# Kernel optimization log

Measured on AMD Instinct MI355X. Metric: run time of the kernel, lower is better.

Reference implementation:

```python
import jax, jax.numpy as jnp
import numpy as np

B, S, D = 4, 2048, 1024
H = 16
HD = D // H
FF = 4096
EPS = 1e-5

def _layernorm(x, g, b):
    mu = jnp.mean(x, axis=-1, keepdims=True)
    var = jnp.mean(jnp.square(x - mu), axis=-1, keepdims=True)
    return (x - mu) * jax.lax.rsqrt(var + EPS) * g + b

def setup_inputs() -> dict:
    key = jax.random.key(0)
    ks = jax.random.split(key, 12)
    s_attn = 1.0 / np.sqrt(D)
    s_ff1 = 1.0 / np.sqrt(D)
    s_ff2 = 1.0 / np.sqrt(FF)
    return {
        "x": jax.random.normal(ks[0], (B, S, D), jnp.float32),
        "ln1_g": jnp.ones((D,), jnp.float32),
        "ln1_b": jnp.zeros((D,), jnp.float32),
        "ln2_g": jnp.ones((D,), jnp.float32),
        "ln2_b": jnp.zeros((D,), jnp.float32),
        "Wq": jax.random.normal(ks[1], (D, D), jnp.float32) * s_attn,
        "Wk": jax.random.normal(ks[2], (D, D), jnp.float32) * s_attn,
        "Wv": jax.random.normal(ks[3], (D, D), jnp.float32) * s_attn,
        "Wo": jax.random.normal(ks[4], (D, D), jnp.float32) * s_attn,
        "W1": jax.random.normal(ks[5], (D, FF), jnp.float32) * s_ff1,
        "b1": jnp.zeros((FF,), jnp.float32),
        "W2": jax.random.normal(ks[6], (FF, D), jnp.float32) * s_ff2,
        "b2": jnp.zeros((D,), jnp.float32),
    }

def reference(x, ln1_g, ln1_b, ln2_g, ln2_b, Wq, Wk, Wv, Wo, W1, b1, W2, b2):
    # pre-LN self-attention (y = x), mask=None, dropout=0, attn proj bias=False
    h = _layernorm(x, ln1_g, ln1_b)                      # [B,S,D]
    q = (h @ Wq).reshape(B, S, H, HD).transpose(0, 2, 1, 3)  # [B,H,S,HD]
    k = (h @ Wk).reshape(B, S, H, HD).transpose(0, 2, 1, 3)
    v = (h @ Wv).reshape(B, S, H, HD).transpose(0, 2, 1, 3)
    scores = jnp.einsum('bhqd,bhkd->bhqk', q, k) / np.sqrt(HD)  # [B,H,S,S]
    attn = jax.nn.softmax(scores, axis=-1)
    o = jnp.einsum('bhqk,bhkd->bhqd', attn, v)           # [B,H,S,HD]
    o = o.transpose(0, 2, 1, 3).reshape(B, S, D) @ Wo
    x = x + o
    h2 = _layernorm(x, ln2_g, ln2_b)
    ff = jax.nn.relu(h2 @ W1 + b1) @ W2 + b2             # note: second FC also has relu per FC default
    ff = jax.nn.relu(ff)
    return x + ff
```

## Files before the change

### kernel.cpp

```cpp
#include <hip/hip_runtime.h>
#include <hip/hip_bf16.h>
#include <cstdint>
#include <cstddef>

typedef unsigned short u16;
typedef unsigned int u32;
typedef __bf16 bf16x2 __attribute__((ext_vector_type(2)));
typedef __bf16 bf16x8 __attribute__((ext_vector_type(8)));
typedef float f32x4 __attribute__((ext_vector_type(4)));

#define NB 4
#define NS 2048
#define ND 1024
#define NH 16
#define NHD 64
#define NFF 4096
#define CSC 0.18033688011112042f

#if __has_builtin(__builtin_amdgcn_exp2f)
#define EXP2(x) __builtin_amdgcn_exp2f(x)
#else
#define EXP2(x) exp2f(x)
#endif

__device__ __forceinline__ u16 f2b(float f) {
  union { bf16x2 h; u32 u; } v;
  v.h[0] = (__bf16)f; v.h[1] = (__bf16)f;
  return (u16)(v.u & 0xFFFF);
}
__device__ __forceinline__ u32 pack2(float a, float b) {
  union { bf16x2 h; u32 u; } v;
  v.h[0] = (__bf16)a; v.h[1] = (__bf16)b;
  return v.u;
}

__device__ __forceinline__ void async_copy16(const u16* g, u16* l) {
  __builtin_amdgcn_global_load_lds(
      (const __attribute__((address_space(1))) void*)(const void*)g,
      (__attribute__((address_space(3))) void*)(void*)l, 16, 0, 0);
}

template <int N> __device__ __forceinline__ void vmw() {
  if constexpr (N == 0) asm volatile("s_waitcnt vmcnt(0)" ::: "memory");
  else if constexpr (N == 6) asm volatile("s_waitcnt vmcnt(6)" ::: "memory");
}

__global__ __launch_bounds__(256) void transpose_f2b(const float* __restrict__ in,
                                                     u16* __restrict__ out,
                                                     int R, int C) {
  __shared__ float tile[32][33];
  const int bx = blockIdx.x * 32;
  const int by = blockIdx.y * 32;
  const int tx = threadIdx.x & 31, ty = threadIdx.x >> 5;
#pragma unroll
  for (int i = 0; i < 32; i += 8)
    tile[ty + i][tx] = in[(size_t)(by + ty + i) * C + bx + tx];
  __syncthreads();
#pragma unroll
  for (int i = 0; i < 32; i += 8)
    out[(size_t)(bx + ty + i) * R + by + tx] = f2b(tile[tx][ty + i]);
}

__global__ __launch_bounds__(256) void ln_kernel(const float* __restrict__ xin,
                                                 const float* __restrict__ g,
                                                 const float* __restrict__ b,
                                                 u16* __restrict__ out) {
  const int row = blockIdx.x;
  const int tid = threadIdx.x;
  const float* p = xin + (size_t)row * ND;
  float v[4];
#pragma unroll
  for (int i = 0; i < 4; i++) v[i] = p[tid + 256 * i];
  float s = 0.f, ss = 0.f;
#pragma unroll
  for (int i = 0; i < 4; i++) { s += v[i]; ss += v[i] * v[i]; }
  for (int off = 32; off > 0; off >>= 1) {
    s += __shfl_down(s, off);
    ss += __shfl_down(ss, off);
  }
  __shared__ float r0[4], r1[4];
  const int w = tid >> 6;
  if ((tid & 63) == 0) { r0[w] = s; r1[w] = ss; }
  __syncthreads();
  s = r0[0] + r0[1] + r0[2] + r0[3];
  ss = r1[0] + r1[1] + r1[2] + r1[3];
  const float mu = s * (1.f / ND);
  const float var = ss * (1.f / ND) - mu * mu;
  const float rstd = rsqrtf(var + 1e-5f);
  u16* o = out + (size_t)row * ND;
#pragma unroll
  for (int i = 0; i < 4; i++) {
    const int c = tid + 256 * i;
    o[c] = f2b((v[i] - mu) * rstd * g[c] + b[c]);
  }
}

template <int OUT_MODE, int RES_MODE, bool BIAS, bool RELU>
__global__ __launch_bounds__(256) void gemm_bt(const u16* __restrict__ A,
                                               const u16* __restrict__ Bt,
                                               const float* __restrict__ bias,
                                               const float* __restrict__ res,
                                               void* __restrict__ out,
                                               u16* __restrict__ outK,
                                               u16* __restrict__ outV,
                                               int M, int N, int K) {
  __shared__ __align__(16) u16 lA[2][128 * 64];
  __shared__ __align__(16) u16 lB[2][128 * 64];
  const int tid = threadIdx.x;
  const int bm = blockIdx.y * 128, bn = blockIdx.x * 128;
  const int w = tid >> 6, lane = tid & 63, quad = lane >> 4, l16 = lane & 15;
  const int wm = (w & 1) * 64, wn = (w >> 1) * 64;
  const int sw = l16 & 7;

  f32x4 acc[4][4];
#pragma unroll
  for (int i = 0; i < 4; i++)
#pragma unroll
    for (int j = 0; j < 4; j++) acc[i][j] = (f32x4){0.f, 0.f, 0.f, 0.f};

  const int srow = w * 8 + (lane >> 3);
  const int sch = (lane & 7) ^ ((lane >> 3) & 7);
  const u16* Ap = A + (size_t)(bm + srow) * K + sch * 8;
  const u16* Bp = Bt + (size_t)(bn + srow) * K + sch * 8;
  const int NT = K >> 6;

#pragma unroll
  for (int c = 0; c < 4; c++)
    async_copy16(Ap + (size_t)c * 32 * K, &lA[0][(c * 32 + w * 8) * 64]);
#pragma unroll
  for (int c = 0; c < 4; c++)
    async_copy16(Bp + (size_t)c * 32 * K, &lB[0][(c * 32 + w * 8) * 64]);

  for (int kt = 0; kt < NT; ++kt) {
    const int cur = kt & 1;
    __syncthreads();
    if (kt + 1 < NT) {
      const size_t koff = (size_t)(kt + 1) * 64;
#pragma unroll
      for (int c = 0; c < 4; c++)
        async_copy16(Ap + (size_t)c * 32 * K + koff,
                     &lA[cur ^ 1][(c * 32 + w * 8) * 64]);
#pragma unroll
      for (int c = 0; c < 4; c++)
        async_copy16(Bp + (size_t)c * 32 * K + koff,
                     &lB[cur ^ 1][(c * 32 + w * 8) * 64]);
    }
    const u16* lAc = lA[cur];
    const u16* lBc = lB[cur];
#pragma unroll
    for (int x = 0; x < 2; x++) {
      bf16x8 af[4], bf[4];
#pragma unroll
      for (int i = 0; i < 4; i++)
        af[i] = *(const bf16x8*)&lAc[(wm + i * 16 + l16) * 64 + ((x * 4 + quad) ^ sw) * 8];
#pragma unroll
      for (int j = 0; j < 4; j++)
        bf[j] = *(const bf16x8*)&lBc[(wn + j * 16 + l16) * 64 + ((x * 4 + quad) ^ sw) * 8];
#pragma unroll
      for (int i = 0; i < 4; i++)
#pragma unroll
        for (int j = 0; j < 4; j++)
          acc[i][j] = __builtin_amdgcn_mfma_f32_16x16x32_bf16(af[i], bf[j], acc[i][j], 0, 0, 0);
    }
  }

  if constexpr (OUT_MODE == 3) {
    const int m0 = bm + wm;
#pragma unroll
    for (int i = 0; i < 4; i++) {
#pragma unroll
      for (int j = 0; j < 4; j++) {
        const int n = bn + wn + j * 16 + l16;
        const int mB = m0 + i * 16 + quad * 4;
        const int bb = mB >> 11, s = mB & 2047;
        if (bn < 1024) {
          const int hh = n >> 6, hd = n & 63;
          u16* o = (u16*)out + (((size_t)(bb * NH + hh) * NS + s) * NHD + hd);
#pragma unroll
          for (int r = 0; r < 4; r++) o[(size_t)r * NHD] = f2b(acc[i][j][r] * CSC);
        } else if (bn < 2048) {
          const int nk = n - 1024;
          const int hh = nk >> 6, hd = nk & 63;
          u16* o = outK + (((size_t)(bb * NH + hh) * NS + s) * NHD + hd);
#pragma unroll
          for (int r = 0; r < 4; r++) o[(size_t)r * NHD] = f2b(acc[i][j][r]);
        } else {
          const int nv = n - 2048;
          const int hh = nv >> 6, hd = nv & 63;
          uint2 pk = make_uint2(pack2(acc[i][j][0], acc[i][j][1]),
                                pack2(acc[i][j][2], acc[i][j][3]));
          *(uint2*)&outV[((size_t)(bb * NH + hh) * NHD + hd) * NS + s] = pk;
        }
      }
    }
  } else {
#pragma unroll
    for (int i = 0; i < 4; i++) {
#pragma unroll
      for (int r = 0; r < 4; r++) {
        const int m = bm + wm + i * 16 + quad * 4 + r;
#pragma unroll
        for (int j = 0; j < 4; j++) {
          const int n = bn + wn + j * 16 + l16;
          float vv = acc[i][j][r];
          if constexpr (BIAS) vv += bias[n];
          if constexpr (RELU) vv = fmaxf(vv, 0.f);
          if constexpr (RES_MODE == 1) vv += res[(size_t)m * N + n];
          if constexpr (OUT_MODE == 0) {
            ((u16*)out)[(size_t)m * N + n] = f2b(vv);
          } else {
            ((float*)out)[(size_t)m * N + n] = vv;
          }
        }
      }
    }
  }
}

template <bool BIAS, bool RELU>
__global__ __launch_bounds__(512, 2) void gemm_8ph(const u16* __restrict__ A,
                                                   const u16* __restrict__ Bt,
                                                   const float* __restrict__ bias,
                                                   u16* __restrict__ out,
                                                   int M, int N, int K) {
  __shared__ __align__(16) u16 lA[2][256 * 64];
  __shared__ __align__(16) u16 lB[2][256 * 64];
  const int tid = threadIdx.x;
  const int w = tid >> 6, lane = tid & 63, quad = lane >> 4, l16 = lane & 15;
  const int sw = l16 & 7;
  const int wr = w >> 2, wc = w & 3;

  const int nb = gridDim.x, chunk = nb >> 3;
  const int wg = ((int)blockIdx.x & 7) * chunk + ((int)blockIdx.x >> 3);
  const int nby = M >> 8;
  const int bx = wg / nby, by = wg % nby;
  const int bm = by * 256, bn = bx * 256;

  f32x4 acc[8][4];
#pragma unroll
  for (int i = 0; i < 8; i++)
#pragma unroll
    for (int j = 0; j < 4; j++) acc[i][j] = (f32x4){0.f, 0.f, 0.f, 0.f};

  const int srow = w * 8 + (lane >> 3);
  const int sch = (lane & 7) ^ ((lane >> 3) & 7);
  const u16* Ap = A + (size_t)(bm + srow) * K + sch * 8;
  const u16* Bp = Bt + (size_t)(bn + srow) * K + sch * 8;
  const int NT = K >> 6;

  auto stA = [&](int t, int h) {
    async_copy16(Ap + (size_t)(h * 64) * K + (size_t)t * 64,
                 &lA[t & 1][(h * 64 + w * 8) * 64]);
  };
  auto stB = [&](int t, int h) {
    async_copy16(Bp + (size_t)(h * 64) * K + (size_t)t * 64,
                 &lB[t & 1][(h * 64 + w * 8) * 64]);
  };

  stA(0, 0); stA(0, 1); stA(0, 2); stA(0, 3);
  stB(0, 0); stB(0, 1); stB(0, 2); stB(0, 3);
  stB(1, 0); stB(1, 1); stB(1, 2); stB(1, 3);
  stA(1, 0); stA(1, 2);
  vmw<6>();
  __builtin_amdgcn_s_barrier();
  __builtin_amdgcn_sched_barrier(0);

  for (int kt = 0; kt < NT; ++kt) {
    const u16* lAc = lA[kt & 1];
    const u16* lBc = lB[kt & 1];
    bf16x8 bfr[4][2];
#pragma unroll
    for (int p = 0; p < 4; ++p) {
      bf16x8 af[2][2];
#pragma unroll
      for (int ii = 0; ii < 2; ii++)
#pragma unroll
        for (int x = 0; x < 2; x++)
          af[ii][x] = *(const bf16x8*)&lAc[(wr * 128 + (p * 2 + ii) * 16 + l16) * 64 +
                                           ((x * 4 + quad) ^ sw) * 8];
      if (p == 0) {
#pragma unroll
        for (int j = 0; j < 4; j++)
#pragma unroll
          for (int x = 0; x < 2; x++)
            bfr[j][x] = *(const bf16x8*)&lBc[(wc * 64 + j * 16 + l16) * 64 +
                                             ((x * 4 + quad) ^ sw) * 8];
        if (kt + 1 < NT) { stA(kt + 1, 1); stA(kt + 1, 3); }
      } else if (p == 1) {
        if (kt + 2 < NT) { stB(kt + 2, 0); stB(kt + 2, 1); }
      } else if (p == 2) {
        if (kt + 2 < NT) { stB(kt + 2, 2); stB(kt + 2, 3); }
      } else {
        if (kt + 2 < NT) { stA(kt + 2, 0); stA(kt + 2, 2); }
      }
      __builtin_amdgcn_s_barrier();
      __builtin_amdgcn_sched_barrier(0);
      __builtin_amdgcn_s_setprio(1);
#pragma unroll
      for (int ii = 0; ii < 2; ii++)
#pragma unroll
        for (int j = 0; j < 4; j++)
#pragma unroll
          for (int x = 0; x < 2; x++)
            acc[p * 2 + ii][j] = __builtin_amdgcn_mfma_f32_16x16x32_bf16(
                af[ii][x], bfr[j][x], acc[p * 2 + ii][j], 0, 0, 0);
      __builtin_amdgcn_s_setprio(0);
      if (p == 3) {
        if (kt + 2 < NT) {
          vmw<6>();
          __builtin_amdgcn_sched_barrier(0);
        } else if (kt + 1 < NT) {
          vmw<0>();
          __builtin_amdgcn_sched_barrier(0);
        }
      }
      __builtin_amdgcn_s_barrier();
      __builtin_amdgcn_sched_barrier(0);
    }
  }

#pragma unroll
  for (int i = 0; i < 8; i++) {
#pragma unroll
    for (int r = 0; r < 4; r++) {
      const int m = bm + wr * 128 + i * 16 + quad * 4 + r;
#pragma unroll
      for (int j = 0; j < 4; j++) {
        const int n = bn + wc * 64 + j * 16 + l16;
        float vv = acc[i][j][r];
        if constexpr (BIAS) vv += bias[n];
        if constexpr (RELU) vv = fmaxf(vv, 0.f);
        out[(size_t)m * N + n] = f2b(vv);
      }
    }
  }
}

#define OSTR 72
__global__ __launch_bounds__(256, 4) void attn_kernel(const u16* __restrict__ Q,
                                                      const u16* __restrict__ K,
                                                      const u16* __restrict__ VT,
                                                      u16* __restrict__ O) {
  __shared__ __align__(16) u16 lK[128 * 64];
  __shared__ __align__(16) u16 lV[64 * 128];
  const int tid = threadIdx.x;
  const int w = tid >> 6, lane = tid & 63, quad = lane >> 4, l16 = lane & 15;
  const int sw = l16 & 7;

  const int bid = blockIdx.x;
  const int xcd = bid & 7, slot = bid >> 3;
  const int bh = xcd + 8 * (slot >> 5);
  const int q0 = (slot & 31) * 64;
  const size_t base = (size_t)bh * NS * NHD;

  const u16* qrow = Q + base + (size_t)(q0 + w * 16 + l16) * NHD;
  bf16x8 qf[2];
  qf[0] = *(const bf16x8*)(qrow + quad * 8);
  qf[1] = *(const bf16x8*)(qrow + 32 + quad * 8);

  const int krow = w * 8 + (lane >> 3);
  const int kch = (lane & 7) ^ ((lane >> 3) & 7);
  const int vrow = w * 4 + (lane >> 4);
  const int vch = (lane & 15) ^ (vrow & 7);
  const u16* kp = K + base + (size_t)krow * 64 + kch * 8;
  const u16* vp = VT + base + (size_t)vrow * NS + vch * 8;

  float l_i = 0.f;
  f32x4 oa[4];
#pragma unroll
  for (int jo = 0; jo < 4; jo++) oa[jo] = (f32x4){0.f, 0.f, 0.f, 0.f};

  for (int kt = 0; kt < NS / 128; ++kt) {
    __syncthreads();
#pragma unroll
    for (int c = 0; c < 4; c++)
      async_copy16(kp + (size_t)c * 32 * 64, &lK[(c * 32 + w * 8) * 64]);
#pragma unroll
    for (int c = 0; c < 4; c++)
      async_copy16(vp + (size_t)c * 16 * NS, &lV[(c * 16 + w * 4) * 128]);
    __syncthreads();
    kp += 128 * 64;
    vp += 128;

    f32x4 sc[8];
#pragma unroll
    for (int j = 0; j < 8; j++) sc[j] = (f32x4){0.f, 0.f, 0.f, 0.f};
#pragma unroll
    for (int x = 0; x < 2; x++)
#pragma unroll
      for (int j = 0; j < 8; j++) {
        bf16x8 kf = *(const bf16x8*)&lK[(j * 16 + l16) * 64 + ((x * 4 + quad) ^ sw) * 8];
        sc[j] = __builtin_amdgcn_mfma_f32_16x16x32_bf16(kf, qf[x], sc[j], 0, 0, 0);
      }

    float rsum = 0.f;
#pragma unroll
    for (int j = 0; j < 8; j++) {
#pragma unroll
      for (int r = 0; r < 4; r++) sc[j][r] = EXP2(sc[j][r]);
      rsum += (sc[j][0] + sc[j][1]) + (sc[j][2] + sc[j][3]);
    }
    rsum += __shfl_xor(rsum, 16);
    rsum += __shfl_xor(rsum, 32);
    l_i += rsum;

#pragma unroll
    for (int x = 0; x < 4; x++) {
      u32 A0 = pack2(sc[2 * x][0], sc[2 * x][1]);
      u32 A1 = pack2(sc[2 * x][2], sc[2 * x][3]);
      u32 B0 = pack2(sc[2 * x + 1][0], sc[2 * x + 1][1]);
      u32 B1 = pack2(sc[2 * x + 1][2], sc[2 * x + 1][3]);
      asm("v_permlane32_swap_b32 %0, %1" : "+v"(A0), "+v"(B0));
      asm("v_permlane32_swap_b32 %0, %1" : "+v"(A1), "+v"(B1));
      asm("v_permlane16_swap_b32 %0, %1" : "+v"(A0), "+v"(B0));
      asm("v_permlane16_swap_b32 %0, %1" : "+v"(A1), "+v"(B1));
      union { u32 u[4]; bf16x8 h; } bq;
      bq.u[0] = A0; bq.u[1] = A1; bq.u[2] = B0; bq.u[3] = B1;
#pragma unroll
      for (int jo = 0; jo < 4; jo++) {
        bf16x8 av = *(const bf16x8*)&lV[(jo * 16 + l16) * 128 + ((x * 4 + quad) ^ sw) * 8];
        oa[jo] = __builtin_amdgcn_mfma_f32_16x16x32_bf16(av, bq.h, oa[jo], 0, 0, 0);
      }
    }
  }

  __syncthreads();
  const float inv = 1.f / l_i;
  u16* lo = &lK[w * 16 * OSTR];
#pragma unroll
  for (int jo = 0; jo < 4; jo++)
#pragma unroll
    for (int pr = 0; pr < 2; pr++)
      *(u32*)&lo[l16 * OSTR + jo * 16 + quad * 4 + pr * 2] =
          pack2(oa[jo][2 * pr] * inv, oa[jo][2 * pr + 1] * inv);

  const int bb = bh >> 4, hh = bh & 15;
#pragma unroll
  for (int t = 0; t < 2; t++) {
    const int row = t * 8 + (lane >> 3);
    const int seg = lane & 7;
    bf16x8 ov = *(const bf16x8*)&lo[row * OSTR + seg * 8];
    const int srow = q0 + w * 16 + row;
    *(int4*)&O[((size_t)bb * NS + srow) * ND + hh * 64 + seg * 8] = *(int4*)&ov;
  }
}

extern "C" void kernel_launch(void* const* d_in, const int* in_sizes, int n_in,
                              void* d_out, int out_size, void* d_ws, size_t ws_size,
                              hipStream_t stream) {
  (void)in_sizes; (void)n_in; (void)out_size; (void)ws_size;
  const float* x = (const float*)d_in[0];
  const float* ln1g = (const float*)d_in[1];
  const float* ln1b = (const float*)d_in[2];
  const float* ln2g = (const float*)d_in[3];
  const float* ln2b = (const float*)d_in[4];
  const float* Wq = (const float*)d_in[5];
  const float* Wk = (const float*)d_in[6];
  const float* Wv = (const float*)d_in[7];
  const float* Wo = (const float*)d_in[8];
  const float* W1 = (const float*)d_in[9];
  const float* b1 = (const float*)d_in[10];
  const float* W2 = (const float*)d_in[11];
  const float* b2 = (const float*)d_in[12];

  u16* ws = (u16*)d_ws;
  u16* h     = ws;
  u16* WqkvT = ws + (size_t)8  * 1048576;
  u16* WoT   = ws + (size_t)11 * 1048576;
  u16* W1T   = ws + (size_t)12 * 1048576;
  u16* W2T   = ws + (size_t)16 * 1048576;
  u16* qb    = ws + (size_t)20 * 1048576;
  u16* kb    = ws + (size_t)28 * 1048576;
  u16* vt    = ws + (size_t)36 * 1048576;
  u16* ob    = ws + (size_t)44 * 1048576;
  float* x2  = (float*)(ws + (size_t)52 * 1048576);
  u16* ff    = qb;
  u16* h2    = h;

  const int M = NB * NS;

  transpose_f2b<<<dim3(32, 32), 256, 0, stream>>>(Wq, WqkvT, ND, ND);
  transpose_f2b<<<dim3(32, 32), 256, 0, stream>>>(Wk, WqkvT + (size_t)1024 * 1024, ND, ND);
  transpose_f2b<<<dim3(32, 32), 256, 0, stream>>>(Wv, WqkvT + (size_t)2048 * 1024, ND, ND);
  transpose_f2b<<<dim3(32, 32), 256, 0, stream>>>(Wo, WoT, ND, ND);
  transpose_f2b<<<dim3(128, 32), 256, 0, stream>>>(W1, W1T, ND, NFF);
  transpose_f2b<<<dim3(32, 128), 256, 0, stream>>>(W2, W2T, NFF, ND);

  ln_kernel<<<M, 256, 0, stream>>>(x, ln1g, ln1b, h);

  gemm_bt<3, 0, false, false><<<dim3(24, 64), 256, 0, stream>>>(
      h, WqkvT, nullptr, nullptr, qb, kb, vt, M, 3072, ND);

  attn_kernel<<<dim3(2048), 256, 0, stream>>>(qb, kb, vt, ob);

  gemm_bt<2, 1, false, false><<<dim3(8, 64), 256, 0, stream>>>(
      ob, WoT, nullptr, x, x2, nullptr, nullptr, M, ND, ND);

  ln_kernel<<<M, 256, 0, stream>>>(x2, ln2g, ln2b, h2);

  gemm_8ph<true, true><<<512, 512, 0, stream>>>(h2, W1T, b1, ff, M, NFF, ND);

  gemm_bt<2, 1, true, true><<<dim3(8, 64), 256, 0, stream>>>(
      ff, W2T, b2, x2, d_out, nullptr, nullptr, M, ND, NFF);
}
```

Baseline: 507.7 us.

## Route all GEMMs through 256x256 eight-phase kernel and merge weight transposes

Removes the simpler 128x128 double-buffered gemm_bt kernel. The QKV, output-projection and FFN2 GEMMs now run on the generalized 256x256 eight-phase pipelined gemm_8ph kernel, which gains the head-split QKV epilogue and residual/fp32 output modes. The four square weight transposes are also merged into one launch. The larger tiles should raise data reuse and MFMA efficiency, but the N=1024 GEMMs only launch 128 blocks, which may underfill the GPU.

After: 567.9 us. +11.9%, slower.

```diff
diff --git a/kernel.cpp b/kernel.cpp
--- a/kernel.cpp
+++ b/kernel.cpp
@@ -43,6 +43,28 @@
 template <int N> __device__ __forceinline__ void vmw() {
   if constexpr (N == 0) asm volatile("s_waitcnt vmcnt(0)" ::: "memory");
   else if constexpr (N == 6) asm volatile("s_waitcnt vmcnt(6)" ::: "memory");
+}
+
+__global__ __launch_bounds__(256) void transpose4_f2b(const float* __restrict__ Wq,
+                                                      const float* __restrict__ Wk,
+                                                      const float* __restrict__ Wv,
+                                                      const float* __restrict__ Wo,
+                                                      u16* __restrict__ WqkvT,
+                                                      u16* __restrict__ WoT) {
+  __shared__ float tile[32][33];
+  const int z = blockIdx.z;
+  const float* in = (z == 0) ? Wq : (z == 1) ? Wk : (z == 2) ? Wv : Wo;
+  u16* out = (z < 3) ? WqkvT + (size_t)z * 1024 * 1024 : WoT;
+  const int bx = blockIdx.x * 32;
+  const int by = blockIdx.y * 32;
+  const int tx = threadIdx.x & 31, ty = threadIdx.x >> 5;
+#pragma unroll
+  for (int i = 0; i < 32; i += 8)
+    tile[ty + i][tx] = in[(size_t)(by + ty + i) * 1024 + bx + tx];
+  __syncthreads();
+#pragma unroll
+  for (int i = 0; i < 32; i += 8)
+    out[(size_t)(bx + ty + i) * 1024 + by + tx] = f2b(tile[tx][ty + i]);
 }
 
 __global__ __launch_bounds__(256) void transpose_f2b(const float* __restrict__ in,
@@ -96,132 +118,13 @@
 }
 
 template <int OUT_MODE, int RES_MODE, bool BIAS, bool RELU>
-__global__ __launch_bounds__(256) void gemm_bt(const u16* __restrict__ A,
-                                               const u16* __restrict__ Bt,
-                                               const float* __restrict__ bias,
-                                               const float* __restrict__ res,
-                                               void* __restrict__ out,
-                                               u16* __restrict__ outK,
-                                               u16* __restrict__ outV,
-                                               int M, int N, int K) {
-  __shared__ __align__(16) u16 lA[2][128 * 64];
-  __shared__ __align__(16) u16 lB[2][128 * 64];
-  const int tid = threadIdx.x;
-  const int bm = blockIdx.y * 128, bn = blockIdx.x * 128;
-  const int w = tid >> 6, lane = tid & 63, quad = lane >> 4, l16 = lane & 15;
-  const int wm = (w & 1) * 64, wn = (w >> 1) * 64;
-  const int sw = l16 & 7;
-
-  f32x4 acc[4][4];
-#pragma unroll
-  for (int i = 0; i < 4; i++)
-#pragma unroll
-    for (int j = 0; j < 4; j++) acc[i][j] = (f32x4){0.f, 0.f, 0.f, 0.f};
-
-  const int srow = w * 8 + (lane >> 3);
-  const int sch = (lane & 7) ^ ((lane >> 3) & 7);
-  const u16* Ap = A + (size_t)(bm + srow) * K + sch * 8;
-  const u16* Bp = Bt + (size_t)(bn + srow) * K + sch * 8;
-  const int NT = K >> 6;
-
-#pragma unroll
-  for (int c = 0; c < 4; c++)
-    async_copy16(Ap + (size_t)c * 32 * K, &lA[0][(c * 32 + w * 8) * 64]);
-#pragma unroll
-  for (int c = 0; c < 4; c++)
-    async_copy16(Bp + (size_t)c * 32 * K, &lB[0][(c * 32 + w * 8) * 64]);
-
-  for (int kt = 0; kt < NT; ++kt) {
-    const int cur = kt & 1;
-    __syncthreads();
-    if (kt + 1 < NT) {
-      const size_t koff = (size_t)(kt + 1) * 64;
-#pragma unroll
-      for (int c = 0; c < 4; c++)
-        async_copy16(Ap + (size_t)c * 32 * K + koff,
-                     &lA[cur ^ 1][(c * 32 + w * 8) * 64]);
-#pragma unroll
-      for (int c = 0; c < 4; c++)
-        async_copy16(Bp + (size_t)c * 32 * K + koff,
-                     &lB[cur ^ 1][(c * 32 + w * 8) * 64]);
-    }
-    const u16* lAc = lA[cur];
-    const u16* lBc = lB[cur];
-#pragma unroll
-    for (int x = 0; x < 2; x++) {
-      bf16x8 af[4], bf[4];
-#pragma unroll
-      for (int i = 0; i < 4; i++)
-        af[i] = *(const bf16x8*)&lAc[(wm + i * 16 + l16) * 64 + ((x * 4 + quad) ^ sw) * 8];
-#pragma unroll
-      for (int j = 0; j < 4; j++)
-        bf[j] = *(const bf16x8*)&lBc[(wn + j * 16 + l16) * 64 + ((x * 4 + quad) ^ sw) * 8];
-#pragma unroll
-      for (int i = 0; i < 4; i++)
-#pragma unroll
-        for (int j = 0; j < 4; j++)
-          acc[i][j] = __builtin_amdgcn_mfma_f32_16x16x32_bf16(af[i], bf[j], acc[i][j], 0, 0, 0);
-    }
-  }
-
-  if constexpr (OUT_MODE == 3) {
-    const int m0 = bm + wm;
-#pragma unroll
-    for (int i = 0; i < 4; i++) {
-#pragma unroll
-      for (int j = 0; j < 4; j++) {
-        const int n = bn + wn + j * 16 + l16;
-        const int mB = m0 + i * 16 + quad * 4;
-        const int bb = mB >> 11, s = mB & 2047;
-        if (bn < 1024) {
-          const int hh = n >> 6, hd = n & 63;
-          u16* o = (u16*)out + (((size_t)(bb * NH + hh) * NS + s) * NHD + hd);
-#pragma unroll
-          for (int r = 0; r < 4; r++) o[(size_t)r * NHD] = f2b(acc[i][j][r] * CSC);
-        } else if (bn < 2048) {
-          const int nk = n - 1024;
-          const int hh = nk >> 6, hd = nk & 63;
-          u16* o = outK + (((size_t)(bb * NH + hh) * NS + s) * NHD + hd);
-#pragma unroll
-          for (int r = 0; r < 4; r++) o[(size_t)r * NHD] = f2b(acc[i][j][r]);
-        } else {
-          const int nv = n - 2048;
-          const int hh = nv >> 6, hd = nv & 63;
-          uint2 pk = make_uint2(pack2(acc[i][j][0], acc[i][j][1]),
-                                pack2(acc[i][j][2], acc[i][j][3]));
-          *(uint2*)&outV[((size_t)(bb * NH + hh) * NHD + hd) * NS + s] = pk;
-        }
-      }
-    }
-  } else {
-#pragma unroll
-    for (int i = 0; i < 4; i++) {
-#pragma unroll
-      for (int r = 0; r < 4; r++) {
-        const int m = bm + wm + i * 16 + quad * 4 + r;
-#pragma unroll
-        for (int j = 0; j < 4; j++) {
-          const int n = bn + wn + j * 16 + l16;
-          float vv = acc[i][j][r];
-          if constexpr (BIAS) vv += bias[n];
-          if constexpr (RELU) vv = fmaxf(vv, 0.f);
-          if constexpr (RES_MODE == 1) vv += res[(size_t)m * N + n];
-          if constexpr (OUT_MODE == 0) {
-            ((u16*)out)[(size_t)m * N + n] = f2b(vv);
-          } else {
-            ((float*)out)[(size_t)m * N + n] = vv;
-          }
-        }
-      }
-    }
-  }
-}
-
-template <bool BIAS, bool RELU>
 __global__ __launch_bounds__(512, 2) void gemm_8ph(const u16* __restrict__ A,
                                                    const u16* __restrict__ Bt,
                                                    const float* __restrict__ bias,
-                                                   u16* __restrict__ out,
+                                                   const float* __restrict__ res,
+                                                   void* __restrict__ out,
+                                                   u16* __restrict__ outK,
+                                                   u16* __restrict__ outV,
                                                    int M, int N, int K) {
   __shared__ __align__(16) u16 lA[2][256 * 64];
   __shared__ __align__(16) u16 lB[2][256 * 64];
@@ -319,18 +222,54 @@
     }
   }
 
-#pragma unroll
-  for (int i = 0; i < 8; i++) {
-#pragma unroll
-    for (int r = 0; r < 4; r++) {
-      const int m = bm + wr * 128 + i * 16 + quad * 4 + r;
+  if constexpr (OUT_MODE == 3) {
+    const int m0 = bm + wr * 128;
+#pragma unroll
+    for (int i = 0; i < 8; i++) {
 #pragma unroll
       for (int j = 0; j < 4; j++) {
         const int n = bn + wc * 64 + j * 16 + l16;
-        float vv = acc[i][j][r];
-        if constexpr (BIAS) vv += bias[n];
-        if constexpr (RELU) vv = fmaxf(vv, 0.f);
-        out[(size_t)m * N + n] = f2b(vv);
+        const int mB = m0 + i * 16 + quad * 4;
+        const int bb = mB >> 11, s = mB & 2047;
+        if (n < 1024) {
+          const int hh = n >> 6, hd = n & 63;
+          u16* o = (u16*)out + (((size_t)(bb * NH + hh) * NS + s) * NHD + hd);
+#pragma unroll
+          for (int r = 0; r < 4; r++) o[(size_t)r * NHD] = f2b(acc[i][j][r] * CSC);
+        } else if (n < 2048) {
+          const int nk = n - 1024;
+          const int hh = nk >> 6, hd = nk & 63;
+          u16* o = outK + (((size_t)(bb * NH + hh) * NS + s) * NHD + hd);
+#pragma unroll
+          for (int r = 0; r < 4; r++) o[(size_t)r * NHD] = f2b(acc[i][j][r]);
+        } else {
+          const int nv = n - 2048;
+          const int hh = nv >> 6, hd = nv & 63;
+          uint2 pk = make_uint2(pack2(acc[i][j][0], acc[i][j][1]),
+                                pack2(acc[i][j][2], acc[i][j][3]));
+          *(uint2*)&outV[((size_t)(bb * NH + hh) * NHD + hd) * NS + s] = pk;
+        }
+      }
+    }
+  } else {
+#pragma unroll
+    for (int i = 0; i < 8; i++) {
+#pragma unroll
+      for (int r = 0; r < 4; r++) {
+        const int m = bm + wr * 128 + i * 16 + quad * 4 + r;
+#pragma unroll
+        for (int j = 0; j < 4; j++) {
+          const int n = bn + wc * 64 + j * 16 + l16;
+          float vv = acc[i][j][r];
+          if constexpr (BIAS) vv += bias[n];
+          if constexpr (RELU) vv = fmaxf(vv, 0.f);
+          if constexpr (RES_MODE == 1) vv += res[(size_t)m * N + n];
+          if constexpr (OUT_MODE == 0) {
+            ((u16*)out)[(size_t)m * N + n] = f2b(vv);
+          } else {
+            ((float*)out)[(size_t)m * N + n] = vv;
+          }
+        }
       }
     }
   }
@@ -479,27 +418,25 @@
 
   const int M = NB * NS;
 
-  transpose_f2b<<<dim3(32, 32), 256, 0, stream>>>(Wq, WqkvT, ND, ND);
-  transpose_f2b<<<dim3(32, 32), 256, 0, stream>>>(Wk, WqkvT + (size_t)1024 * 1024, ND, ND);
-  transpose_f2b<<<dim3(32, 32), 256, 0, stream>>>(Wv, WqkvT + (size_t)2048 * 1024, ND, ND);
-  transpose_f2b<<<dim3(32, 32), 256, 0, stream>>>(Wo, WoT, ND, ND);
+  transpose4_f2b<<<dim3(32, 32, 4), 256, 0, stream>>>(Wq, Wk, Wv, Wo, WqkvT, WoT);
   transpose_f2b<<<dim3(128, 32), 256, 0, stream>>>(W1, W1T, ND, NFF);
   transpose_f2b<<<dim3(32, 128), 256, 0, stream>>>(W2, W2T, NFF, ND);
 
   ln_kernel<<<M, 256, 0, stream>>>(x, ln1g, ln1b, h);
 
-  gemm_bt<3, 0, false, false><<<dim3(24, 64), 256, 0, stream>>>(
+  gemm_8ph<3, 0, false, false><<<384, 512, 0, stream>>>(
       h, WqkvT, nullptr, nullptr, qb, kb, vt, M, 3072, ND);
 
   attn_kernel<<<dim3(2048), 256, 0, stream>>>(qb, kb, vt, ob);
 
-  gemm_bt<2, 1, false, false><<<dim3(8, 64), 256, 0, stream>>>(
+  gemm_8ph<2, 1, false, false><<<128, 512, 0, stream>>>(
       ob, WoT, nullptr, x, x2, nullptr, nullptr, M, ND, ND);
 
   ln_kernel<<<M, 256, 0, stream>>>(x2, ln2g, ln2b, h2);
 
-  gemm_8ph<true, true><<<512, 512, 0, stream>>>(h2, W1T, b1, ff, M, NFF, ND);
-
-  gemm_bt<2, 1, true, true><<<dim3(8, 64), 256, 0, stream>>>(
+  gemm_8ph<0, 0, true, true><<<512, 512, 0, stream>>>(
+      h2, W1T, b1, nullptr, ff, nullptr, nullptr, M, NFF, ND);
+
+  gemm_8ph<2, 1, true, true><<<128, 512, 0, stream>>>(
       ff, W2T, b2, x2, d_out, nullptr, nullptr, M, ND, NFF);
 }
```
